# Performance work log

Measured on AMD Instinct MI355X. Metric: run time of the kernel, lower is better.

## Reference

```python
import jax, jax.numpy as jnp
import numpy as np

B = 8388608
AGE_MAX = 120.0
INV_SQRT_PI = 1.0 / np.sqrt(np.pi).astype(np.float32)
INV_SQRT_2PI = 1.0 / np.sqrt(2.0 * np.pi).astype(np.float32)


def _ndtr(z):
    # standard normal CDF via erf
    return 0.5 * (1.0 + jax.lax.erf(z * np.float32(1.0 / np.sqrt(2.0))))


def _I_norm(mu, sigma2, y):
    # Faithful translation of CRPS.I_norm (closed-form CRPS of Normal(mu, s) at y)
    s = jnp.sqrt(sigma2)
    ystd = (y - mu) / s
    ncdf = _ndtr(ystd)                              # Normal(mu,s).cdf(y)
    npdf = jnp.exp(-0.5 * ystd * ystd) * INV_SQRT_2PI / s  # Normal(mu,s).pdf(y)
    n2cdf = _ndtr(ystd * np.float32(np.sqrt(2.0)))  # Normal(mu, s/sqrt(2)).cdf(y)
    return s * (ystd * ncdf * ncdf + 2.0 * ncdf * npdf * s - INV_SQRT_PI * n2cdf)


def setup_inputs() -> dict:
    key = jax.random.key(0)
    k1, k2, k3 = jax.random.split(key, 3)
    pred_params = jax.random.normal(k1, (B, 2), dtype=jnp.float32)  # [mu, log_sigma2]
    tgts = jax.random.uniform(k2, (B, 2), dtype=jnp.float32, minval=1e-3, maxval=1.0)  # [tte, censor]
    ages = jax.random.uniform(k3, (B,), dtype=jnp.float32, minval=0.0, maxval=1.0)
    return {"pred_params": pred_params, "tgts": tgts, "ages": ages, "use_intvl": 1}


def reference(pred_params, tgts, ages, use_intvl):
    mu = pred_params[:, 0]
    sigma2 = jnp.exp(pred_params[:, 1])  # s.exp() in original
    tte = tgts[:, 0]
    censor = tgts[:, 1]
    max_tte = AGE_MAX - ages
    Y = jnp.log(tte)       # time.log() / log(e)
    T = jnp.log(max_tte)

    I = lambda y: _I_norm(mu, sigma2, y)
    I_ = lambda y: _I_norm(-mu, sigma2, y)

    if use_intvl:
        crps = I(Y) + I_(-T) + (1.0 - censor) * (I_(-Y) - I_(-T))
    else:
        crps = I(Y) + (1.0 - censor) * I_(-Y)
    return jnp.sum(crps) / np.float32(B)
```

## Files before the change

### kernel.cpp

```cpp
#include <hip/hip_runtime.h>
#include <math.h>


#define AGE_MAX_F      120.0f
#define INV_SQRT_PI_F  0.5641895835477563f
#define INV_SQRT_2PI_F 0.3989422804014327f
#define SQRT_2PI_F     2.5066282746310002f
#define SQRT_2_F       1.4142135623730951f

#define NBLOCKS 2048
#define NTHREADS 256

__device__ __forceinline__ float ndtr_from_pdf(float z, float phi) {
    const float za = fabsf(z);
    const float t  = __builtin_amdgcn_rcpf(fmaf(0.2316419f, za, 1.0f));
    float p = fmaf(1.330274429f, t, -1.821255978f);
    p = fmaf(p, t, 1.781477937f);
    p = fmaf(p, t, -0.356563782f);
    p = fmaf(p, t, 0.319381530f);
    p = p * t;
    const float hm = fmaf(-phi, p, 0.5f);
    return fmaf(copysignf(1.0f, z), hm, 0.5f);
}

__device__ __forceinline__ float crps_elem(float mu, float ls, float tte,
                                           float cen, float age, int use_intvl) {
    const float s     = __expf( 0.5f * ls);
    const float inv_s = __expf(-0.5f * ls);
    const float Y     = __logf(tte);

    const float dy   = Y - mu;
    const float z    = dy * inv_s;
    const float pdf  = __expf(-0.5f * z * z) * INV_SQRT_2PI_F;
    const float c    = ndtr_from_pdf(z, pdf);
    const float pdf2 = pdf * pdf * SQRT_2PI_F;
    const float c2   = ndtr_from_pdf(z * SQRT_2_F, pdf2);

    const float sp  = s * INV_SQRT_PI_F;
    const float tp  = 2.0f * s * pdf;
    const float IY  = dy * c * c + tp * c - sp * c2;
    const float omc = 1.0f - c;
    const float InY = -dy * omc * omc + tp * omc - sp * (1.0f - c2);

    if (use_intvl) {
        const float T     = __logf(AGE_MAX_F - age);
        const float dt    = mu - T;
        const float zt    = dt * inv_s;
        const float pdft  = __expf(-0.5f * zt * zt) * INV_SQRT_2PI_F;
        const float ct    = ndtr_from_pdf(zt, pdft);
        const float pdft2 = pdft * pdft * SQRT_2PI_F;
        const float c2t   = ndtr_from_pdf(zt * SQRT_2_F, pdft2);
        const float InT   = dt * ct * ct + 2.0f * s * ct * pdft - sp * c2t;
        return IY + InT + (1.0f - cen) * (InY - InT);
    } else {
        return IY + (1.0f - cen) * InY;
    }
}

__device__ __forceinline__ float crps_pair(float4 p, float4 t, float2 a, int ui) {
    return crps_elem(p.x, p.y, t.x, t.y, a.x, ui)
         + crps_elem(p.z, p.w, t.z, t.w, a.y, ui);
}

template <bool USE_ATOMIC>
__global__ __launch_bounds__(NTHREADS, 4) void crps_kernel(
    const float4* __restrict__ pp,
    const float4* __restrict__ tg,
    const float2* __restrict__ ag,
    const int*    __restrict__ use_intvl_p,
    float*        __restrict__ partials,
    int npairs, float inv_total)
{
    const int tid    = blockIdx.x * blockDim.x + threadIdx.x;
    const int stride = gridDim.x * blockDim.x;
    const int ui     = *use_intvl_p;

    float acc = 0.0f;

    int i = tid;
    for (; i + 3 * stride < npairs; i += 4 * stride) {
        float4 p[4], t[4];
        float2 a[4];
        #pragma unroll
        for (int u = 0; u < 4; ++u) {
            const int idx = i + u * stride;
            p[u] = pp[idx];
            t[u] = tg[idx];
            a[u] = ag[idx];
        }
        float s0 = crps_pair(p[0], t[0], a[0], ui);
        float s1 = crps_pair(p[1], t[1], a[1], ui);
        float s2 = crps_pair(p[2], t[2], a[2], ui);
        float s3 = crps_pair(p[3], t[3], a[3], ui);
        acc += (s0 + s1) + (s2 + s3);
    }
    for (; i < npairs; i += stride) {
        acc += crps_pair(pp[i], tg[i], ag[i], ui);
    }

    #pragma unroll
    for (int off = 32; off > 0; off >>= 1)
        acc += __shfl_down(acc, off);

    __shared__ float wsum[NTHREADS / 64];
    const int lane = threadIdx.x & 63;
    const int wid  = threadIdx.x >> 6;
    if (lane == 0) wsum[wid] = acc;
    __syncthreads();
    if (threadIdx.x == 0) {
        float blocksum = 0.0f;
        #pragma unroll
        for (int w = 0; w < NTHREADS / 64; ++w) blocksum += wsum[w];
        if (USE_ATOMIC) {
            atomicAdd(partials, blocksum * inv_total);
        } else {
            partials[blockIdx.x] = blocksum;
        }
    }
}

__global__ __launch_bounds__(256) void reduce_kernel(
    const float4* __restrict__ partials,
    float* __restrict__ out, float inv_total)
{
    float acc = 0.0f;
    #pragma unroll
    for (int u = 0; u < 2; ++u) {
        const float4 v = partials[threadIdx.x + u * 256];
        acc += (v.x + v.y) + (v.z + v.w);
    }
    #pragma unroll
    for (int off = 32; off > 0; off >>= 1)
        acc += __shfl_down(acc, off);

    __shared__ float wsum[4];
    const int lane = threadIdx.x & 63;
    const int wid  = threadIdx.x >> 6;
    if (lane == 0) wsum[wid] = acc;
    __syncthreads();
    if (threadIdx.x == 0) {
        out[0] = ((wsum[0] + wsum[1]) + (wsum[2] + wsum[3])) * inv_total;
    }
}

extern "C" void kernel_launch(void* const* d_in, const int* in_sizes, int n_in,
                              void* d_out, int out_size, void* d_ws, size_t ws_size,
                              hipStream_t stream) {
    const float4* pp = (const float4*)d_in[0];
    const float4* tg = (const float4*)d_in[1];
    const float2* ag = (const float2*)d_in[2];
    const int*    ui = (const int*)d_in[3];
    float* out = (float*)d_out;

    const int n      = in_sizes[2];
    const int npairs = n >> 1;
    const float inv_total = 1.0f / (float)n;

    if (ws_size >= NBLOCKS * sizeof(float)) {
        float* partials = (float*)d_ws;
        crps_kernel<false><<<NBLOCKS, NTHREADS, 0, stream>>>(
            pp, tg, ag, ui, partials, npairs, inv_total);
        reduce_kernel<<<1, 256, 0, stream>>>(
            (const float4*)partials, out, inv_total);
    } else {
        hipMemsetAsync(d_out, 0, sizeof(float), stream);
        crps_kernel<true><<<NBLOCKS, NTHREADS, 0, stream>>>(
            pp, tg, ag, ui, out, npairs, inv_total);
    }
}
```

Measured before the change: 178.8 us.

## Replace grid-stride loop with one-shot grid of two pairs per thread

Drops the persistent grid-stride loop and launches enough blocks so that each thread processes exactly two float4 pairs, one from each half of the array. The reduce kernel is generalized to sum a variable number of partials with 1024 threads. The occupancy hint in launch_bounds is removed. This aims to raise wave-level parallelism and cut loop overhead, at the cost of more blocks, more partials to reduce, and less per-thread ILP.

```diff
diff --git a/kernel.cpp b/kernel.cpp
--- a/kernel.cpp
+++ b/kernel.cpp
@@ -8,7 +8,6 @@
 #define SQRT_2PI_F     2.5066282746310002f
 #define SQRT_2_F       1.4142135623730951f
 
-#define NBLOCKS 2048
 #define NTHREADS 256
 
 __device__ __forceinline__ float ndtr_from_pdf(float z, float phi) {
@@ -63,7 +62,7 @@
 }
 
 template <bool USE_ATOMIC>
-__global__ __launch_bounds__(NTHREADS, 4) void crps_kernel(
+__global__ __launch_bounds__(NTHREADS) void crps_kernel(
     const float4* __restrict__ pp,
     const float4* __restrict__ tg,
     const float2* __restrict__ ag,
@@ -71,31 +70,24 @@
     float*        __restrict__ partials,
     int npairs, float inv_total)
 {
-    const int tid    = blockIdx.x * blockDim.x + threadIdx.x;
-    const int stride = gridDim.x * blockDim.x;
-    const int ui     = *use_intvl_p;
+    const int half = gridDim.x * NTHREADS;
+    const int i0   = blockIdx.x * NTHREADS + threadIdx.x;
+    const int i1   = i0 + half;
+    const int ui   = *use_intvl_p;
 
     float acc = 0.0f;
-
-    int i = tid;
-    for (; i + 3 * stride < npairs; i += 4 * stride) {
-        float4 p[4], t[4];
-        float2 a[4];
-        #pragma unroll
-        for (int u = 0; u < 4; ++u) {
-            const int idx = i + u * stride;
-            p[u] = pp[idx];
-            t[u] = tg[idx];
-            a[u] = ag[idx];
+    if (i0 < npairs) {
+        const float4 p0 = pp[i0];
+        const float4 t0 = tg[i0];
+        const float2 a0 = ag[i0];
+        if (i1 < npairs) {
+            const float4 p1 = pp[i1];
+            const float4 t1 = tg[i1];
+            const float2 a1 = ag[i1];
+            acc = crps_pair(p0, t0, a0, ui) + crps_pair(p1, t1, a1, ui);
+        } else {
+            acc = crps_pair(p0, t0, a0, ui);
         }
-        float s0 = crps_pair(p[0], t[0], a[0], ui);
-        float s1 = crps_pair(p[1], t[1], a[1], ui);
-        float s2 = crps_pair(p[2], t[2], a[2], ui);
-        float s3 = crps_pair(p[3], t[3], a[3], ui);
-        acc += (s0 + s1) + (s2 + s3);
-    }
-    for (; i < npairs; i += stride) {
-        acc += crps_pair(pp[i], tg[i], ag[i], ui);
     }
 
     #pragma unroll
@@ -119,27 +111,28 @@
     }
 }
 
-__global__ __launch_bounds__(256) void reduce_kernel(
-    const float4* __restrict__ partials,
-    float* __restrict__ out, float inv_total)
+__global__ __launch_bounds__(1024) void reduce_kernel(
+    const float* __restrict__ partials,
+    float* __restrict__ out, int nparts, float inv_total)
 {
     float acc = 0.0f;
-    #pragma unroll
-    for (int u = 0; u < 2; ++u) {
-        const float4 v = partials[threadIdx.x + u * 256];
-        acc += (v.x + v.y) + (v.z + v.w);
-    }
+    for (int i = threadIdx.x; i < nparts; i += 1024)
+        acc += partials[i];
+
     #pragma unroll
     for (int off = 32; off > 0; off >>= 1)
         acc += __shfl_down(acc, off);
 
-    __shared__ float wsum[4];
+    __shared__ float wsum[16];
     const int lane = threadIdx.x & 63;
     const int wid  = threadIdx.x >> 6;
     if (lane == 0) wsum[wid] = acc;
     __syncthreads();
     if (threadIdx.x == 0) {
-        out[0] = ((wsum[0] + wsum[1]) + (wsum[2] + wsum[3])) * inv_total;
+        float s = 0.0f;
+        #pragma unroll
+        for (int w = 0; w < 16; ++w) s += wsum[w];
+        out[0] = s * inv_total;
     }
 }
 
@@ -156,15 +149,16 @@
     const int npairs = n >> 1;
     const float inv_total = 1.0f / (float)n;
 
-    if (ws_size >= NBLOCKS * sizeof(float)) {
+    int blocks = (npairs + 2 * NTHREADS - 1) / (2 * NTHREADS);
+
+    if (ws_size >= (size_t)blocks * sizeof(float)) {
         float* partials = (float*)d_ws;
-        crps_kernel<false><<<NBLOCKS, NTHREADS, 0, stream>>>(
+        crps_kernel<false><<<blocks, NTHREADS, 0, stream>>>(
             pp, tg, ag, ui, partials, npairs, inv_total);
-        reduce_kernel<<<1, 256, 0, stream>>>(
-            (const float4*)partials, out, inv_total);
+        reduce_kernel<<<1, 1024, 0, stream>>>(partials, out, blocks, inv_total);
     } else {
         hipMemsetAsync(d_out, 0, sizeof(float), stream);
-        crps_kernel<true><<<NBLOCKS, NTHREADS, 0, stream>>>(
+        crps_kernel<true><<<blocks, NTHREADS, 0, stream>>>(
             pp, tg, ag, ui, out, npairs, inv_total);
     }
 }
```

New measurement: 176.0 us. About the same (-1.5%).
